# Kernel optimization log

Hardware: AMD Instinct MI355X
Metric: run time of the kernel (lower is better)

The kernel has to match this reference:

```python
import math
import jax, jax.numpy as jnp
import numpy as np

N_HEADS = 16
HIDDEN = 1024
FACTOR = 256
N_DK = HIDDEN // N_HEADS
B, S = 4, 2048


def _linear_params(key, fan_in, fan_out):
    kw, kb = jax.random.split(key)
    bound = 1.0 / math.sqrt(fan_in)
    W = jax.random.uniform(kw, (fan_in, fan_out), jnp.float32, -bound, bound)
    b = jax.random.uniform(kb, (fan_out,), jnp.float32, -bound, bound)
    return W, b


def setup_inputs() -> dict:
    key = jax.random.key(0)
    ks = jax.random.split(key, 12)
    inp = {
        "query": jax.random.normal(ks[0], (B, S, HIDDEN), jnp.float32),
        "key": jax.random.normal(ks[1], (B, S, HIDDEN), jnp.float32),
        "value": jax.random.normal(ks[2], (B, S, HIDDEN), jnp.float32),
        "mask": jax.random.randint(ks[3], (B, S), 0, 2, jnp.int32),
    }
    names = [("pq", HIDDEN, FACTOR), ("tq", FACTOR, HIDDEN),
             ("pk", HIDDEN, FACTOR), ("tk", FACTOR, HIDDEN),
             ("pv", HIDDEN, FACTOR), ("tv", FACTOR, HIDDEN),
             ("po", HIDDEN, FACTOR), ("to", FACTOR, HIDDEN)]
    for i, (nm, fi, fo) in enumerate(names):
        W, b = _linear_params(ks[4 + i], fi, fo)
        inp[f"W{nm}"], inp[f"b{nm}"] = W, b
    return inp


def _factored(x, Wp, bp, Wt, bt):
    # proj -> leaky_relu(0.2) -> tran
    h = jax.nn.leaky_relu(x @ Wp + bp, negative_slope=0.2)
    return h @ Wt + bt


def reference(query, key, value, mask,
              Wpq, bpq, Wtq, btq, Wpk, bpk, Wtk, btk,
              Wpv, bpv, Wtv, btv, Wpo, bpo, Wto, bto):
    bsize = query.shape[0]

    def split_heads(x):  # [B,S,H*Dk] -> [B,H,S,Dk]
        return x.reshape(bsize, -1, N_HEADS, N_DK).transpose(0, 2, 1, 3)

    q = split_heads(_factored(query, Wpq, bpq, Wtq, btq))
    k = split_heads(_factored(key, Wpk, bpk, Wtk, btk))
    v = split_heads(_factored(value, Wpv, bpv, Wtv, btv))

    scores = jnp.einsum("bhqd,bhkd->bhqk", q, k) / math.sqrt(N_DK)
    m = (mask == 0)[:, None, None, :]  # [B,1,1,S]
    scores = jnp.where(m, jnp.float32(-1e20), scores)
    attn = jax.nn.softmax(scores, axis=-1)
    cv = jnp.einsum("bhqk,bhkd->bhqd", attn, v)
    cv = cv.transpose(0, 2, 1, 3).reshape(bsize, -1, N_HEADS * N_DK)
    # dropout omitted (eval mode / deterministic reference)
    return _factored(cv, Wpo, bpo, Wto, bto)
```

## Files before the change

### kernel.cpp

```cpp
#include <hip/hip_runtime.h>
#include <cstdint>
#include <cstddef>

typedef __bf16 bf16_t;
typedef __bf16 bf16x8 __attribute__((ext_vector_type(8)));
typedef float  f32x4  __attribute__((ext_vector_type(4)));
typedef unsigned int uint32x4 __attribute__((ext_vector_type(4)));

#define DEV_INLINE __device__ __forceinline__

constexpr int Bsz = 4, Ssz = 2048, HID = 1024, FAC = 256, NH = 16, DKc = 64;
constexpr int Mrows = Bsz * Ssz;
constexpr float QSCALE = 0.18033688011112042f;

struct Ptr8 { const float* p[8]; };
struct Ptr3 { const float* p[3]; };

DEV_INLINE float fast_exp2(float x) {
#if __has_builtin(__builtin_amdgcn_exp2f)
  return __builtin_amdgcn_exp2f(x);
#else
  return exp2f(x);
#endif
}

DEV_INLINE void async16(const void* g, void* l) {
  __builtin_amdgcn_global_load_lds((const __attribute__((address_space(1))) void*)g,
                                   (__attribute__((address_space(3))) void*)l, 16, 0, 0);
}

DEV_INLINE int SW(int r) { return (r & 3) | ((r >> 1) & 4); }

__global__ __launch_bounds__(256) void k_prep_w(Ptr8 s, bf16_t* wpt, bf16_t* wtt) {
  const int z = blockIdx.z;
  const int K = (z < 4) ? HID : FAC;
  const int N = (z < 4) ? FAC : HID;
  if ((int)(blockIdx.x * 32) >= N || (int)(blockIdx.y * 32) >= K) return;
  __shared__ float t[32][33];
  const float* src = s.p[z];
  bf16_t* dst = (z < 4) ? (wpt + (size_t)z * FAC * HID) : (wtt + (size_t)(z - 4) * FAC * HID);
  const int tx = threadIdx.x & 31, ty = threadIdx.x >> 5;
  const int kb = blockIdx.y * 32, nb = blockIdx.x * 32;
#pragma unroll
  for (int j = 0; j < 4; ++j)
    t[ty + j * 8][tx] = src[(size_t)(kb + ty + j * 8) * N + nb + tx];
  __syncthreads();
#pragma unroll
  for (int j = 0; j < 4; ++j)
    dst[(size_t)(nb + ty + j * 8) * K + kb + tx] = (bf16_t)t[tx][ty + j * 8];
}

__global__ __launch_bounds__(256) void k_pack_bias(Ptr8 s, const int* __restrict__ mask,
                                                   float* bp, float* bt, float* mf, bf16_t* mb) {
  const int i = blockIdx.x * 256 + threadIdx.x;
  if (i < 4 * FAC) bp[i] = s.p[i >> 8][i & 255];
  if (i < 4 * HID) bt[i] = s.p[4 + (i >> 10)][i & 1023];
  if (i < Bsz * Ssz) {
    const float m = (mask[i] != 0) ? 1.f : 0.f;
    mf[i] = m;
    mb[i] = (bf16_t)m;
  }
}

__global__ __launch_bounds__(256) void k_tv(const bf16_t* __restrict__ src, bf16_t* __restrict__ dst) {
  constexpr int LDT = 72;
  __shared__ __align__(16) bf16_t T[64 * LDT];
  const int st = blockIdx.x, h = blockIdx.y, b = blockIdx.z;
  const int tid = threadIdx.x;
  const int sr = tid >> 3, sc8 = (tid & 7) * 8;
  const size_t g0 = (size_t)(b * Ssz + st * 64 + sr) * HID + h * DKc + sc8;
  *(uint32x4*)(T + sr * LDT + sc8) = *(const uint32x4*)(src + g0);
  *(uint32x4*)(T + (sr + 32) * LDT + sc8) = *(const uint32x4*)(src + g0 + (size_t)32 * HID);
  __syncthreads();
  union { bf16_t e[8]; uint32x4 u; } o0, o1;
#pragma unroll
  for (int j = 0; j < 8; ++j) {
    o0.e[j] = T[(sc8 + j) * LDT + sr];
    o1.e[j] = T[(sc8 + j) * LDT + sr + 32];
  }
  const size_t d0 = ((size_t)(b * NH + h) * DKc + sr) * Ssz + st * 64 + sc8;
  *(uint32x4*)(dst + d0) = o0.u;
  *(uint32x4*)(dst + d0 + (size_t)32 * Ssz) = o1.u;
}

template <int CAST_A, typename OUT_T>
__global__ __launch_bounds__(256) void k_gemmP(Ptr3 Asrc,
                                               const bf16_t* __restrict__ Aall,
                                               const bf16_t* __restrict__ Bt_,
                                               const float* __restrict__ biasAll,
                                               OUT_T* __restrict__ Call,
                                               int K,
                                               long long Az, long long Bz, long long Cz, int biasz) {
  constexpr int LDTA = CAST_A ? 40 : 32;
  __shared__ __align__(16) bf16_t As[2][64 * LDTA];
  __shared__ __align__(16) bf16_t Bs[2][128 * 32];

  const int z = blockIdx.z;
  const bf16_t* Bt = Bt_ + (size_t)z * Bz;
  const float* bias = biasAll + (size_t)z * biasz;
  OUT_T* C = Call + (size_t)z * Cz;

  const int tid = threadIdx.x;
  const int lane = tid & 63, wave = tid >> 6;
  const int quad = lane >> 4, l16 = lane & 15;
  const int m0 = blockIdx.y * 64, n0 = blockIdx.x * 128;

  const int arow = wave * 16 + (lane >> 2), akc = (lane & 3) * 8;
  const bf16_t* gB0 = Bt + (size_t)(n0 + arow) * K + akc;
  const bf16_t* gB1 = gB0 + (size_t)64 * K;

  const float* gAf = nullptr;
  const bf16_t* gA = nullptr;
  const int crow = tid >> 2, chalf = (tid & 3) * 8;
  if (CAST_A) gAf = Asrc.p[z] + (size_t)(m0 + crow) * K + chalf;
  else        gA  = Aall + (size_t)z * Az + (size_t)(m0 + arow) * K + akc;

  async16(gB0, Bs[0] + wave * 512);
  async16(gB1, Bs[0] + 2048 + wave * 512);
  if (CAST_A) {
    f32x4 x0 = *(const f32x4*)gAf;
    f32x4 x1 = *(const f32x4*)(gAf + 4);
    union { bf16_t h[8]; uint32x4 u; } o;
#pragma unroll
    for (int j = 0; j < 4; ++j) { o.h[j] = (bf16_t)x0[j]; o.h[4 + j] = (bf16_t)x1[j]; }
    *(uint32x4*)(As[0] + crow * LDTA + chalf) = o.u;
  } else {
    async16(gA, As[0] + wave * 512);
  }

  f32x4 acc[4][2] = {};
  const int nk = K / 32;

  for (int it = 0; it < nk; ++it) {
    const int cur = it & 1, nxt = cur ^ 1;
    __syncthreads();

    f32x4 xa, xb;
    const int k1 = (it + 1) * 32;
    if (it + 1 < nk) {
      async16(gB0 + k1, Bs[nxt] + wave * 512);
      async16(gB1 + k1, Bs[nxt] + 2048 + wave * 512);
      if (CAST_A) {
        xa = *(const f32x4*)(gAf + k1);
        xb = *(const f32x4*)(gAf + k1 + 4);
      } else {
        async16(gA + k1, As[nxt] + wave * 512);
      }
    }

    bf16x8 af[4], bfr[2];
#pragma unroll
    for (int i = 0; i < 4; ++i)
      af[i] = *(const bf16x8*)(As[cur] + (i * 16 + l16) * LDTA + quad * 8);
#pragma unroll
    for (int i = 0; i < 2; ++i)
      bfr[i] = *(const bf16x8*)(Bs[cur] + (wave * 32 + i * 16 + l16) * 32 + quad * 8);
#pragma unroll
    for (int mi = 0; mi < 4; ++mi)
#pragma unroll
      for (int ni = 0; ni < 2; ++ni)
        acc[mi][ni] = __builtin_amdgcn_mfma_f32_16x16x32_bf16(af[mi], bfr[ni], acc[mi][ni], 0, 0, 0);

    if (CAST_A && it + 1 < nk) {
      union { bf16_t h[8]; uint32x4 u; } o;
#pragma unroll
      for (int j = 0; j < 4; ++j) { o.h[j] = (bf16_t)xa[j]; o.h[4 + j] = (bf16_t)xb[j]; }
      *(uint32x4*)(As[nxt] + crow * LDTA + chalf) = o.u;
    }
  }

#pragma unroll
  for (int mi = 0; mi < 4; ++mi) {
    const int rbase = m0 + mi * 16 + quad * 4;
#pragma unroll
    for (int ni = 0; ni < 2; ++ni) {
      const int col = n0 + wave * 32 + ni * 16 + l16;
      const float bv = bias[col];
#pragma unroll
      for (int r = 0; r < 4; ++r) {
        float y = acc[mi][ni][r] + bv;
        y = (y > 0.f) ? y : 0.2f * y;
        C[(size_t)(rbase + r) * FAC + col] = (OUT_T)y;
      }
    }
  }
}

template <int ACT, int RM, typename OUT_T>
__global__ __launch_bounds__(256) void k_gemm(const bf16_t* __restrict__ Aall,
                                              const bf16_t* __restrict__ Btall,
                                              const float* __restrict__ biasAll,
                                              OUT_T* __restrict__ Call,
                                              OUT_T* __restrict__ C2,
                                              const float* __restrict__ rowmul,
                                              int N, int K,
                                              long long Az, long long Bz, long long Cz, int biasz,
                                              float sc0, float sc1, float sc2) {
  __shared__ __align__(16) bf16_t As[128 * 32];
  __shared__ __align__(16) bf16_t Bs[128 * 32];

  const int z = blockIdx.z;
  const bf16_t* Bt = Btall + (size_t)z * Bz;
  const float* bias = biasAll + (size_t)z * biasz;
  OUT_T* C = (z == 2 && C2) ? C2 : (Call + (size_t)z * Cz);
  const float scale = (z == 0) ? sc0 : ((z == 1) ? sc1 : sc2);

  const int tid = threadIdx.x;
  const int lane = tid & 63, wave = tid >> 6;
  const int quad = lane >> 4, l16 = lane & 15;
  const int wr = wave >> 1, wc = wave & 1;
  const int m0 = blockIdx.y * 128, n0 = blockIdx.x * 128;

  const int arow = wave * 16 + (lane >> 2), akc = (lane & 3) * 8;
  const bf16_t* gB0 = Bt + (size_t)(n0 + arow) * K + akc;
  const bf16_t* gB1 = gB0 + (size_t)64 * K;
  bf16_t* lB0 = Bs + wave * 512;
  bf16_t* lB1 = Bs + 2048 + wave * 512;

  const bf16_t* A = Aall + (size_t)z * Az;
  const bf16_t* gA0 = A + (size_t)(m0 + arow) * K + akc;
  const bf16_t* gA1 = gA0 + (size_t)64 * K;
  bf16_t* lA0 = As + wave * 512;
  bf16_t* lA1 = As + 2048 + wave * 512;

  f32x4 acc[4][4] = {};

  for (int k0 = 0; k0 < K; k0 += 32) {
    async16(gB0 + k0, lB0);
    async16(gB1 + k0, lB1);
    async16(gA0 + k0, lA0);
    async16(gA1 + k0, lA1);
    __syncthreads();

    bf16x8 af[4], bfr[4];
#pragma unroll
    for (int i = 0; i < 4; ++i)
      af[i] = *(const bf16x8*)(As + (wr * 64 + i * 16 + l16) * 32 + quad * 8);
#pragma unroll
    for (int i = 0; i < 4; ++i)
      bfr[i] = *(const bf16x8*)(Bs + (wc * 64 + i * 16 + l16) * 32 + quad * 8);
#pragma unroll
    for (int mi = 0; mi < 4; ++mi)
#pragma unroll
      for (int ni = 0; ni < 4; ++ni)
        acc[mi][ni] = __builtin_amdgcn_mfma_f32_16x16x32_bf16(af[mi], bfr[ni], acc[mi][ni], 0, 0, 0);
    if (k0 + 32 < K) __syncthreads();
  }

#pragma unroll
  for (int mi = 0; mi < 4; ++mi) {
    const int rbase = m0 + wr * 64 + mi * 16 + quad * 4;
    float rmv[4] = {1.f, 1.f, 1.f, 1.f};
    if (RM && z == 2) {
#pragma unroll
      for (int r = 0; r < 4; ++r) rmv[r] = rowmul[rbase + r];
    }
#pragma unroll
    for (int ni = 0; ni < 4; ++ni) {
      const int col = n0 + wc * 64 + ni * 16 + l16;
      const float bv = bias[col];
#pragma unroll
      for (int r = 0; r < 4; ++r) {
        float y = acc[mi][ni][r] + bv;
        if (ACT == 1) y = (y > 0.f) ? y : 0.2f * y;
        y *= scale * rmv[r];
        C[(size_t)(rbase + r) * N + col] = (OUT_T)y;
      }
    }
  }
}

__global__ __launch_bounds__(256, 4) void k_attn(const bf16_t* __restrict__ qkv,
                                                 const bf16_t* __restrict__ mb,
                                                 bf16_t* __restrict__ cv) {
  __shared__ __align__(16) bf16_t Ks[2][64 * 64];
  __shared__ __align__(16) bf16_t Vt[2][64 * 64];
  __shared__ __align__(16) bf16_t Ml[Ssz];

  const int qt = blockIdx.x, h = blockIdx.y, b = blockIdx.z;
  const bf16_t* qp = qkv;
  const bf16_t* kp = qkv + (size_t)Mrows * HID;
  const bf16_t* vtp = qkv + 2 * (size_t)Mrows * HID + (size_t)(b * NH + h) * DKc * Ssz;

  const int tid = threadIdx.x;
  const int lane = tid & 63, wave = tid >> 6;
  const int quad = lane >> 4, l16 = lane & 15;

  const int r0 = wave * 16 + (lane >> 3);
  const int r1 = r0 + 8;
  const int c0 = ((lane & 7) ^ SW(r0)) * 8;
  const int c1 = ((lane & 7) ^ SW(r1)) * 8;
  const int ldsOff = wave * 1024;
  const bf16_t* kgA = kp + (size_t)(b * Ssz + r0) * HID + h * DKc + c0;
  const bf16_t* kgB = kp + (size_t)(b * Ssz + r1) * HID + h * DKc + c1;
  const bf16_t* vgA = vtp + (size_t)r0 * Ssz + c0;
  const bf16_t* vgB = vtp + (size_t)r1 * Ssz + c1;

  *(uint32x4*)(Ml + tid * 8) = *(const uint32x4*)(mb + (size_t)b * Ssz + tid * 8);
  async16(kgA, Ks[0] + ldsOff);
  async16(kgB, Ks[0] + ldsOff + 512);
  async16(vgA, Vt[0] + ldsOff);
  async16(vgB, Vt[0] + ldsOff + 512);

  bf16x8 aq0[2], aq1[2];
#pragma unroll
  for (int g = 0; g < 2; ++g) {
    const size_t qrow = (size_t)(b * Ssz + qt * 128 + g * 64 + wave * 16 + l16) * HID + h * DKc + quad * 8;
    aq0[g] = *(const bf16x8*)(qp + qrow);
    aq1[g] = *(const bf16x8*)(qp + qrow + 32);
  }
  __syncthreads();

  const int krow = 8 * (l16 >> 2) + (l16 & 3);
  f32x4 acc[2][4] = {};
  f32x4 dacc[2] = {};
  const bf16x8 zfrag = {};

  for (int kt = 0; kt < 32; ++kt) {
    const int cur = kt & 1, nxt = cur ^ 1;
    if (kt < 31) {
      const size_t ko = (size_t)(kt + 1) * 64 * HID;
      const int vo = (kt + 1) * 64;
      async16(kgA + ko, Ks[nxt] + ldsOff);
      async16(kgB + ko, Ks[nxt] + ldsOff + 512);
      async16(vgA + vo, Vt[nxt] + ldsOff);
      async16(vgB + vo, Vt[nxt] + ldsOff + 512);
    }

    uint32_t pk[2][8];
    constexpr int koff[4] = {0, 4, 32, 36};
#pragma unroll
    for (int ks = 0; ks < 4; ++ks) {
      const int row = krow + koff[ks];
      const int sw = SW(row);
      bf16x8 a0 = *(const bf16x8*)(Ks[cur] + row * 64 + (quad ^ sw) * 8);
      bf16x8 a1 = *(const bf16x8*)(Ks[cur] + row * 64 + ((quad + 4) ^ sw) * 8);
#pragma unroll
      for (int g = 0; g < 2; ++g) {
        f32x4 c = {};
        c = __builtin_amdgcn_mfma_f32_16x16x32_bf16(a0, aq0[g], c, 0, 0, 0);
        c = __builtin_amdgcn_mfma_f32_16x16x32_bf16(a1, aq1[g], c, 0, 0, 0);
        union { bf16_t h[2]; uint32_t u; } p01, p23;
        p01.h[0] = (bf16_t)fast_exp2(c[0]);
        p01.h[1] = (bf16_t)fast_exp2(c[1]);
        p23.h[0] = (bf16_t)fast_exp2(c[2]);
        p23.h[1] = (bf16_t)fast_exp2(c[3]);
        pk[g][ks * 2] = p01.u;
        pk[g][ks * 2 + 1] = p23.u;
      }
    }
    union { uint32x4 u; bf16x8 h; } ap0[2], ap1[2];
#pragma unroll
    for (int g = 0; g < 2; ++g) {
      ap0[g].u = uint32x4{pk[g][0], pk[g][1], pk[g][2], pk[g][3]};
      ap1[g].u = uint32x4{pk[g][4], pk[g][5], pk[g][6], pk[g][7]};
    }

    bf16x8 mr0 = *(const bf16x8*)(Ml + kt * 64 + quad * 8);
    bf16x8 mr1 = *(const bf16x8*)(Ml + kt * 64 + 32 + quad * 8);
    if (l16 != 0) { mr0 = zfrag; mr1 = zfrag; }
#pragma unroll
    for (int g = 0; g < 2; ++g) {
      dacc[g] = __builtin_amdgcn_mfma_f32_16x16x32_bf16(ap0[g].h, mr0, dacc[g], 0, 0, 0);
      dacc[g] = __builtin_amdgcn_mfma_f32_16x16x32_bf16(ap1[g].h, mr1, dacc[g], 0, 0, 0);
    }

#pragma unroll
    for (int d = 0; d < 4; ++d) {
      const int row = d * 16 + l16;
      const int sw = SW(row);
      bf16x8 bv0 = *(const bf16x8*)(Vt[cur] + row * 64 + (quad ^ sw) * 8);
      bf16x8 bv1 = *(const bf16x8*)(Vt[cur] + row * 64 + ((quad + 4) ^ sw) * 8);
#pragma unroll
      for (int g = 0; g < 2; ++g) {
        acc[g][d] = __builtin_amdgcn_mfma_f32_16x16x32_bf16(ap0[g].h, bv0, acc[g][d], 0, 0, 0);
        acc[g][d] = __builtin_amdgcn_mfma_f32_16x16x32_bf16(ap1[g].h, bv1, acc[g][d], 0, 0, 0);
      }
    }

    __syncthreads();
  }

#pragma unroll
  for (int g = 0; g < 2; ++g) {
    const size_t obase = (size_t)(b * Ssz + qt * 128 + g * 64 + wave * 16 + quad * 4) * HID + h * DKc + l16;
#pragma unroll
    for (int r = 0; r < 4; ++r) {
      const float denom = __shfl(dacc[g][r], lane & 48, 64);
      const float rl = 1.f / denom;
#pragma unroll
      for (int d = 0; d < 4; ++d)
        cv[obase + (size_t)r * HID + d * 16] = (bf16_t)(acc[g][d][r] * rl);
    }
  }
}

extern "C" void kernel_launch(void* const* d_in, const int* in_sizes, int n_in,
                              void* d_out, int out_size, void* d_ws, size_t ws_size,
                              hipStream_t stream) {
  (void)in_sizes; (void)n_in; (void)out_size; (void)ws_size;
  const float* q_in = (const float*)d_in[0];
  const float* k_in = (const float*)d_in[1];
  const float* v_in = (const float*)d_in[2];
  const int* mask = (const int*)d_in[3];

  bf16_t* XB = (bf16_t*)d_ws;
  bf16_t* H3 = XB + (size_t)3 * Mrows * HID;
  bf16_t* CV = H3 + (size_t)3 * Mrows * FAC;
  bf16_t* WPT = CV + (size_t)Mrows * HID;
  bf16_t* WTT = WPT + (size_t)4 * FAC * HID;
  float* BP = (float*)(WTT + (size_t)4 * FAC * HID);
  float* BT = BP + 4 * FAC;
  float* MF = BT + 4 * HID;
  bf16_t* MB = (bf16_t*)(MF + Mrows);
  bf16_t* VTg = XB + 2 * (size_t)Mrows * HID;

  Ptr8 w;
  w.p[0] = (const float*)d_in[4];  w.p[1] = (const float*)d_in[8];
  w.p[2] = (const float*)d_in[12]; w.p[3] = (const float*)d_in[16];
  w.p[4] = (const float*)d_in[6];  w.p[5] = (const float*)d_in[10];
  w.p[6] = (const float*)d_in[14]; w.p[7] = (const float*)d_in[18];
  hipLaunchKernelGGL(k_prep_w, dim3(32, 32, 8), dim3(256), 0, stream, w, WPT, WTT);

  Ptr8 bs;
  bs.p[0] = (const float*)d_in[5];  bs.p[1] = (const float*)d_in[9];
  bs.p[2] = (const float*)d_in[13]; bs.p[3] = (const float*)d_in[17];
  bs.p[4] = (const float*)d_in[7];  bs.p[5] = (const float*)d_in[11];
  bs.p[6] = (const float*)d_in[15]; bs.p[7] = (const float*)d_in[19];
  hipLaunchKernelGGL(k_pack_bias, dim3(64), dim3(256), 0, stream, bs, mask, BP, BT, MF, MB);

  Ptr3 xs; xs.p[0] = q_in; xs.p[1] = k_in; xs.p[2] = v_in;
  Ptr3 nullp; nullp.p[0] = nullp.p[1] = nullp.p[2] = nullptr;

  hipLaunchKernelGGL((k_gemmP<1, bf16_t>), dim3(2, Mrows / 64, 3), dim3(256), 0, stream,
                     xs, (const bf16_t*)nullptr, WPT, BP, H3,
                     HID, 0LL, (long long)FAC * HID, (long long)Mrows * FAC, FAC);

  hipLaunchKernelGGL((k_gemm<0, 1, bf16_t>), dim3(HID / 128, Mrows / 128, 3), dim3(256), 0, stream,
                     H3, WTT, BT, XB, CV, MF,
                     HID, FAC, (long long)Mrows * FAC, (long long)FAC * HID, (long long)Mrows * HID, HID,
                     QSCALE, 1.f, 1.f);

  hipLaunchKernelGGL(k_tv, dim3(Ssz / 64, NH, Bsz), dim3(256), 0, stream, CV, VTg);

  hipLaunchKernelGGL(k_attn, dim3(Ssz / 128, NH, Bsz), dim3(256), 0, stream, XB, MB, CV);

  hipLaunchKernelGGL((k_gemmP<0, bf16_t>), dim3(2, Mrows / 64, 1), dim3(256), 0, stream,
                     nullp, CV, WPT + (size_t)3 * FAC * HID, BP + 3 * FAC, H3,
                     HID, 0LL, 0LL, 0LL, 0);

  hipLaunchKernelGGL((k_gemm<0, 0, float>), dim3(HID / 128, Mrows / 128, 1), dim3(256), 0, stream,
                     H3, WTT + (size_t)3 * FAC * HID, BT + 3 * HID, (float*)d_out, (float*)nullptr,
                     (const float*)nullptr, HID, FAC, 0LL, 0LL, 0LL, 0, 1.f, 1.f, 1.f);
}
```

Measured before the change: 353.6 us.

## Fuse V transpose into GEMM epilogue, merge prep kernels, enlarge attention query tile

The V projection GEMM now writes its masked output directly in the transposed [B,H,Dk,S] layout, which removes the separate transpose kernel and its round-trip through global memory. The weight-prep and bias/mask-pack kernels are merged into one launch. The attention kernel now handles 256 query rows per block instead of 128, so each K/V tile loaded into LDS is reused across more queries. The price is more registers (launch bounds drop to 2 blocks per CU), half as many attention blocks, and transposed-output stores in the GEMM that are only 8 bytes wide and strided.

```diff
diff --git a/kernel.cpp b/kernel.cpp
--- a/kernel.cpp
+++ b/kernel.cpp
@@ -6,6 +6,7 @@
 typedef __bf16 bf16x8 __attribute__((ext_vector_type(8)));
 typedef float  f32x4  __attribute__((ext_vector_type(4)));
 typedef unsigned int uint32x4 __attribute__((ext_vector_type(4)));
+typedef unsigned int uint32x2 __attribute__((ext_vector_type(2)));
 
 #define DEV_INLINE __device__ __forceinline__
 
@@ -31,13 +32,28 @@
 
 DEV_INLINE int SW(int r) { return (r & 3) | ((r >> 1) & 4); }
 
-__global__ __launch_bounds__(256) void k_prep_w(Ptr8 s, bf16_t* wpt, bf16_t* wtt) {
+__global__ __launch_bounds__(256) void k_prep(Ptr8 w, Ptr8 bsrc, const int* __restrict__ mask,
+                                              bf16_t* wpt, bf16_t* wtt,
+                                              float* bp, float* bt, float* mf, bf16_t* mb) {
   const int z = blockIdx.z;
+  if (z == 8) {
+    const int bid = blockIdx.y * 32 + blockIdx.x;
+    if (bid >= 64) return;
+    const int i = bid * 256 + threadIdx.x;
+    if (i < 4 * FAC) bp[i] = bsrc.p[i >> 8][i & 255];
+    if (i < 4 * HID) bt[i] = bsrc.p[4 + (i >> 10)][i & 1023];
+    if (i < Bsz * Ssz) {
+      const float m = (mask[i] != 0) ? 1.f : 0.f;
+      mf[i] = m;
+      mb[i] = (bf16_t)m;
+    }
+    return;
+  }
   const int K = (z < 4) ? HID : FAC;
   const int N = (z < 4) ? FAC : HID;
   if ((int)(blockIdx.x * 32) >= N || (int)(blockIdx.y * 32) >= K) return;
   __shared__ float t[32][33];
-  const float* src = s.p[z];
+  const float* src = w.p[z];
   bf16_t* dst = (z < 4) ? (wpt + (size_t)z * FAC * HID) : (wtt + (size_t)(z - 4) * FAC * HID);
   const int tx = threadIdx.x & 31, ty = threadIdx.x >> 5;
   const int kb = blockIdx.y * 32, nb = blockIdx.x * 32;
@@ -48,39 +64,6 @@
 #pragma unroll
   for (int j = 0; j < 4; ++j)
     dst[(size_t)(nb + ty + j * 8) * K + kb + tx] = (bf16_t)t[tx][ty + j * 8];
-}
-
-__global__ __launch_bounds__(256) void k_pack_bias(Ptr8 s, const int* __restrict__ mask,
-                                                   float* bp, float* bt, float* mf, bf16_t* mb) {
-  const int i = blockIdx.x * 256 + threadIdx.x;
-  if (i < 4 * FAC) bp[i] = s.p[i >> 8][i & 255];
-  if (i < 4 * HID) bt[i] = s.p[4 + (i >> 10)][i & 1023];
-  if (i < Bsz * Ssz) {
-    const float m = (mask[i] != 0) ? 1.f : 0.f;
-    mf[i] = m;
-    mb[i] = (bf16_t)m;
-  }
-}
-
-__global__ __launch_bounds__(256) void k_tv(const bf16_t* __restrict__ src, bf16_t* __restrict__ dst) {
-  constexpr int LDT = 72;
-  __shared__ __align__(16) bf16_t T[64 * LDT];
-  const int st = blockIdx.x, h = blockIdx.y, b = blockIdx.z;
-  const int tid = threadIdx.x;
-  const int sr = tid >> 3, sc8 = (tid & 7) * 8;
-  const size_t g0 = (size_t)(b * Ssz + st * 64 + sr) * HID + h * DKc + sc8;
-  *(uint32x4*)(T + sr * LDT + sc8) = *(const uint32x4*)(src + g0);
-  *(uint32x4*)(T + (sr + 32) * LDT + sc8) = *(const uint32x4*)(src + g0 + (size_t)32 * HID);
-  __syncthreads();
-  union { bf16_t e[8]; uint32x4 u; } o0, o1;
-#pragma unroll
-  for (int j = 0; j < 8; ++j) {
-    o0.e[j] = T[(sc8 + j) * LDT + sr];
-    o1.e[j] = T[(sc8 + j) * LDT + sr + 32];
-  }
-  const size_t d0 = ((size_t)(b * NH + h) * DKc + sr) * Ssz + st * 64 + sc8;
-  *(uint32x4*)(dst + d0) = o0.u;
-  *(uint32x4*)(dst + d0 + (size_t)32 * Ssz) = o1.u;
 }
 
 template <int CAST_A, typename OUT_T>
@@ -186,24 +169,24 @@
   }
 }
 
-template <int ACT, int RM, typename OUT_T>
+template <int TVW, typename OUT_T>
 __global__ __launch_bounds__(256) void k_gemm(const bf16_t* __restrict__ Aall,
                                               const bf16_t* __restrict__ Btall,
                                               const float* __restrict__ biasAll,
                                               OUT_T* __restrict__ Call,
-                                              OUT_T* __restrict__ C2,
+                                              bf16_t* __restrict__ C2,
                                               const float* __restrict__ rowmul,
                                               int N, int K,
                                               long long Az, long long Bz, long long Cz, int biasz,
-                                              float sc0, float sc1, float sc2) {
+                                              float sc0, float sc1) {
   __shared__ __align__(16) bf16_t As[128 * 32];
   __shared__ __align__(16) bf16_t Bs[128 * 32];
 
   const int z = blockIdx.z;
   const bf16_t* Bt = Btall + (size_t)z * Bz;
   const float* bias = biasAll + (size_t)z * biasz;
-  OUT_T* C = (z == 2 && C2) ? C2 : (Call + (size_t)z * Cz);
-  const float scale = (z == 0) ? sc0 : ((z == 1) ? sc1 : sc2);
+  OUT_T* C = Call + (size_t)z * Cz;
+  const float scale = (z == 0) ? sc0 : sc1;
 
   const int tid = threadIdx.x;
   const int lane = tid & 63, wave = tid >> 6;
@@ -247,30 +230,45 @@
     if (k0 + 32 < K) __syncthreads();
   }
 
+  if (TVW && z == 2) {
+#pragma unroll
+    for (int mi = 0; mi < 4; ++mi) {
+      const int rbase = m0 + wr * 64 + mi * 16 + quad * 4;
+      const int bb = rbase >> 11, s = rbase & 2047;
+      float rmv[4];
+#pragma unroll
+      for (int r = 0; r < 4; ++r) rmv[r] = rowmul[rbase + r];
+#pragma unroll
+      for (int ni = 0; ni < 4; ++ni) {
+        const int col = n0 + wc * 64 + ni * 16 + l16;
+        const float bv = bias[col];
+        const int h = col >> 6, d = col & 63;
+        union { bf16_t e[4]; uint32x2 u; } p;
+#pragma unroll
+        for (int r = 0; r < 4; ++r) p.e[r] = (bf16_t)((acc[mi][ni][r] + bv) * rmv[r]);
+        *(uint32x2*)(C2 + (((size_t)((bb * NH + h) * DKc + d)) << 11) + s) = p.u;
+      }
+    }
+    return;
+  }
+
 #pragma unroll
   for (int mi = 0; mi < 4; ++mi) {
     const int rbase = m0 + wr * 64 + mi * 16 + quad * 4;
-    float rmv[4] = {1.f, 1.f, 1.f, 1.f};
-    if (RM && z == 2) {
-#pragma unroll
-      for (int r = 0; r < 4; ++r) rmv[r] = rowmul[rbase + r];
-    }
 #pragma unroll
     for (int ni = 0; ni < 4; ++ni) {
       const int col = n0 + wc * 64 + ni * 16 + l16;
       const float bv = bias[col];
 #pragma unroll
       for (int r = 0; r < 4; ++r) {
-        float y = acc[mi][ni][r] + bv;
-        if (ACT == 1) y = (y > 0.f) ? y : 0.2f * y;
-        y *= scale * rmv[r];
+        float y = (acc[mi][ni][r] + bv) * scale;
         C[(size_t)(rbase + r) * N + col] = (OUT_T)y;
       }
     }
   }
 }
 
-__global__ __launch_bounds__(256, 4) void k_attn(const bf16_t* __restrict__ qkv,
+__global__ __launch_bounds__(256, 2) void k_attn(const bf16_t* __restrict__ qkv,
                                                  const bf16_t* __restrict__ mb,
                                                  bf16_t* __restrict__ cv) {
   __shared__ __align__(16) bf16_t Ks[2][64 * 64];
@@ -302,18 +300,18 @@
   async16(vgA, Vt[0] + ldsOff);
   async16(vgB, Vt[0] + ldsOff + 512);
 
-  bf16x8 aq0[2], aq1[2];
-#pragma unroll
-  for (int g = 0; g < 2; ++g) {
-    const size_t qrow = (size_t)(b * Ssz + qt * 128 + g * 64 + wave * 16 + l16) * HID + h * DKc + quad * 8;
+  bf16x8 aq0[4], aq1[4];
+#pragma unroll
+  for (int g = 0; g < 4; ++g) {
+    const size_t qrow = (size_t)(b * Ssz + qt * 256 + g * 64 + wave * 16 + l16) * HID + h * DKc + quad * 8;
     aq0[g] = *(const bf16x8*)(qp + qrow);
     aq1[g] = *(const bf16x8*)(qp + qrow + 32);
   }
   __syncthreads();
 
   const int krow = 8 * (l16 >> 2) + (l16 & 3);
-  f32x4 acc[2][4] = {};
-  f32x4 dacc[2] = {};
+  f32x4 acc[4][4] = {};
+  f32x4 dacc[4] = {};
   const bf16x8 zfrag = {};
 
   for (int kt = 0; kt < 32; ++kt) {
@@ -327,7 +325,7 @@
       async16(vgB + vo, Vt[nxt] + ldsOff + 512);
     }
 
-    uint32_t pk[2][8];
+    union U { uint32x4 u; bf16x8 h; } ap0[4], ap1[4];
     constexpr int koff[4] = {0, 4, 32, 36};
 #pragma unroll
     for (int ks = 0; ks < 4; ++ks) {
@@ -336,7 +334,7 @@
       bf16x8 a0 = *(const bf16x8*)(Ks[cur] + row * 64 + (quad ^ sw) * 8);
       bf16x8 a1 = *(const bf16x8*)(Ks[cur] + row * 64 + ((quad + 4) ^ sw) * 8);
 #pragma unroll
-      for (int g = 0; g < 2; ++g) {
+      for (int g = 0; g < 4; ++g) {
         f32x4 c = {};
         c = __builtin_amdgcn_mfma_f32_16x16x32_bf16(a0, aq0[g], c, 0, 0, 0);
         c = __builtin_amdgcn_mfma_f32_16x16x32_bf16(a1, aq1[g], c, 0, 0, 0);
@@ -345,22 +343,17 @@
         p01.h[1] = (bf16_t)fast_exp2(c[1]);
         p23.h[0] = (bf16_t)fast_exp2(c[2]);
         p23.h[1] = (bf16_t)fast_exp2(c[3]);
-        pk[g][ks * 2] = p01.u;
-        pk[g][ks * 2 + 1] = p23.u;
-      }
-    }
-    union { uint32x4 u; bf16x8 h; } ap0[2], ap1[2];
-#pragma unroll
-    for (int g = 0; g < 2; ++g) {
-      ap0[g].u = uint32x4{pk[g][0], pk[g][1], pk[g][2], pk[g][3]};
-      ap1[g].u = uint32x4{pk[g][4], pk[g][5], pk[g][6], pk[g][7]};
+        U& t = (ks < 2) ? ap0[g] : ap1[g];
+        t.u[(ks & 1) * 2] = p01.u;
+        t.u[(ks & 1) * 2 + 1] = p23.u;
+      }
     }
 
     bf16x8 mr0 = *(const bf16x8*)(Ml + kt * 64 + quad * 8);
     bf16x8 mr1 = *(const bf16x8*)(Ml + kt * 64 + 32 + quad * 8);
     if (l16 != 0) { mr0 = zfrag; mr1 = zfrag; }
 #pragma unroll
-    for (int g = 0; g < 2; ++g) {
+    for (int g = 0; g < 4; ++g) {
       dacc[g] = __builtin_amdgcn_mfma_f32_16x16x32_bf16(ap0[g].h, mr0, dacc[g], 0, 0, 0);
       dacc[g] = __builtin_amdgcn_mfma_f32_16x16x32_bf16(ap1[g].h, mr1, dacc[g], 0, 0, 0);
     }
@@ -372,7 +365,7 @@
       bf16x8 bv0 = *(const bf16x8*)(Vt[cur] + row * 64 + (quad ^ sw) * 8);
       bf16x8 bv1 = *(const bf16x8*)(Vt[cur] + row * 64 + ((quad + 4) ^ sw) * 8);
 #pragma unroll
-      for (int g = 0; g < 2; ++g) {
+      for (int g = 0; g < 4; ++g) {
         acc[g][d] = __builtin_amdgcn_mfma_f32_16x16x32_bf16(ap0[g].h, bv0, acc[g][d], 0, 0, 0);
         acc[g][d] = __builtin_amdgcn_mfma_f32_16x16x32_bf16(ap1[g].h, bv1, acc[g][d], 0, 0, 0);
       }
@@ -382,8 +375,8 @@
   }
 
 #pragma unroll
-  for (int g = 0; g < 2; ++g) {
-    const size_t obase = (size_t)(b * Ssz + qt * 128 + g * 64 + wave * 16 + quad * 4) * HID + h * DKc + l16;
+  for (int g = 0; g < 4; ++g) {
+    const size_t obase = (size_t)(b * Ssz + qt * 256 + g * 64 + wave * 16 + quad * 4) * HID + h * DKc + l16;
 #pragma unroll
     for (int r = 0; r < 4; ++r) {
       const float denom = __shfl(dacc[g][r], lane & 48, 64);
@@ -420,14 +413,13 @@
   w.p[2] = (const float*)d_in[12]; w.p[3] = (const float*)d_in[16];
   w.p[4] = (const float*)d_in[6];  w.p[5] = (const float*)d_in[10];
   w.p[6] = (const float*)d_in[14]; w.p[7] = (const float*)d_in[18];
-  hipLaunchKernelGGL(k_prep_w, dim3(32, 32, 8), dim3(256), 0, stream, w, WPT, WTT);
-
   Ptr8 bs;
   bs.p[0] = (const float*)d_in[5];  bs.p[1] = (const float*)d_in[9];
   bs.p[2] = (const float*)d_in[13]; bs.p[3] = (const float*)d_in[17];
   bs.p[4] = (const float*)d_in[7];  bs.p[5] = (const float*)d_in[11];
   bs.p[6] = (const float*)d_in[15]; bs.p[7] = (const float*)d_in[19];
-  hipLaunchKernelGGL(k_pack_bias, dim3(64), dim3(256), 0, stream, bs, mask, BP, BT, MF, MB);
+  hipLaunchKernelGGL(k_prep, dim3(32, 32, 9), dim3(256), 0, stream, w, bs, mask,
+                     WPT, WTT, BP, BT, MF, MB);
 
   Ptr3 xs; xs.p[0] = q_in; xs.p[1] = k_in; xs.p[2] = v_in;
   Ptr3 nullp; nullp.p[0] = nullp.p[1] = nullp.p[2] = nullptr;
@@ -436,20 +428,18 @@
                      xs, (const bf16_t*)nullptr, WPT, BP, H3,
                      HID, 0LL, (long long)FAC * HID, (long long)Mrows * FAC, FAC);
 
-  hipLaunchKernelGGL((k_gemm<0, 1, bf16_t>), dim3(HID / 128, Mrows / 128, 3), dim3(256), 0, stream,
-                     H3, WTT, BT, XB, CV, MF,
+  hipLaunchKernelGGL((k_gemm<1, bf16_t>), dim3(HID / 128, Mrows / 128, 3), dim3(256), 0, stream,
+                     H3, WTT, BT, XB, VTg, MF,
                      HID, FAC, (long long)Mrows * FAC, (long long)FAC * HID, (long long)Mrows * HID, HID,
-                     QSCALE, 1.f, 1.f);
-
-  hipLaunchKernelGGL(k_tv, dim3(Ssz / 64, NH, Bsz), dim3(256), 0, stream, CV, VTg);
-
-  hipLaunchKernelGGL(k_attn, dim3(Ssz / 128, NH, Bsz), dim3(256), 0, stream, XB, MB, CV);
+                     QSCALE, 1.f);
+
+  hipLaunchKernelGGL(k_attn, dim3(Ssz / 256, NH, Bsz), dim3(256), 0, stream, XB, MB, CV);
 
   hipLaunchKernelGGL((k_gemmP<0, bf16_t>), dim3(2, Mrows / 64, 1), dim3(256), 0, stream,
                      nullp, CV, WPT + (size_t)3 * FAC * HID, BP + 3 * FAC, H3,
                      HID, 0LL, 0LL, 0LL, 0);
 
-  hipLaunchKernelGGL((k_gemm<0, 0, float>), dim3(HID / 128, Mrows / 128, 1), dim3(256), 0, stream,
-                     H3, WTT + (size_t)3 * FAC * HID, BT + 3 * HID, (float*)d_out, (float*)nullptr,
-                     (const float*)nullptr, HID, FAC, 0LL, 0LL, 0LL, 0, 1.f, 1.f, 1.f);
-}
+  hipLaunchKernelGGL((k_gemm<0, float>), dim3(HID / 128, Mrows / 128, 1), dim3(256), 0, stream,
+                     H3, WTT + (size_t)3 * FAC * HID, BT + 3 * HID, (float*)d_out, (bf16_t*)nullptr,
+                     (const float*)nullptr, HID, FAC, 0LL, 0LL, 0LL, 0, 1.f, 1.f);
+}
```

Measured after the change: 344.2 us. 2.7% less time.
